# Performance work log

Hardware: AMD Instinct MI355X
Metric: run time of the kernel (lower is better)

## Reference

```python
import jax, jax.numpy as jnp
import numpy as np

KEY_DIM = 64
SCALE_PER_SEQ = 1.0 / np.sqrt(KEY_DIM).astype(np.float32)   # attn_scale_factor_per_seq default
SCALE_OVER_SEQS = 1.0 / np.sqrt(KEY_DIM).astype(np.float32) # attn_scale_factor_over_seqs default


def setup_inputs() -> dict:
    key = jax.random.key(0)
    ks = jax.random.split(key, 6)
    b, i, t, j, d = 8, 256, 64, 256, 256
    kd, vd = KEY_DIM, 64
    return {
        "input_seq": jax.random.normal(ks[0], (b, i, d), dtype=jnp.float32),
        "memory_x": jax.random.normal(ks[1], (b, t, j, d), dtype=jnp.float32),
        "memory_y": jax.random.normal(ks[2], (b, t, j, d), dtype=jnp.float32),
        "Wq": jax.random.normal(ks[3], (d, kd), dtype=jnp.float32) * (1.0 / np.sqrt(d)),
        "bq": jnp.zeros((kd,), dtype=jnp.float32),
        "Wk": jax.random.normal(ks[4], (d, kd), dtype=jnp.float32) * (1.0 / np.sqrt(d)),
        "bk": jnp.zeros((kd,), dtype=jnp.float32),
        "Wv": jax.random.normal(ks[5], (d, vd), dtype=jnp.float32) * (1.0 / np.sqrt(d)),
        "bv": jnp.zeros((vd,), dtype=jnp.float32),
    }


def reference(input_seq, memory_x, memory_y, Wq, bq, Wk, bk, Wv, bv):
    # Dense projections
    queries = input_seq @ Wq + bq            # [b, i, kd]
    keys = memory_x @ Wk + bk                # [b, t, j, kd]
    values = memory_y @ Wv + bv              # [b, t, j, vd]

    # Raw scores between every query and every token of every memory sequence
    attn_mat = jnp.einsum('bik,btjk->btij', queries, keys)  # [b, t, i, j]

    # Level 1: within-sequence attention (softmax over tokens j)
    per_seq_attn = jax.nn.softmax(SCALE_PER_SEQ * attn_mat, axis=-1)
    per_seq_retrieved = jnp.einsum('btij,btjk->btik', per_seq_attn, values)  # [b, t, i, vd]

    # Level 2: over-sequences attention (max over j, softmax over t)
    mem_seq_scores = jnp.max(attn_mat, axis=-1)                      # [b, t, i]
    mem_seq_attn = jax.nn.softmax(SCALE_OVER_SEQS * mem_seq_scores, axis=1)

    retrieved_mems = jnp.einsum('bti,btik->bik', mem_seq_attn, per_seq_retrieved)  # [b, i, vd]
    return retrieved_mems
```

## Files before the change

kernel.cpp:

```cpp
#include <hip/hip_runtime.h>
#include <hip/hip_bf16.h>

#define NB 8
#define NT 64
#define NI 256
#define NJ 256
#define ND 256
#define NKD 64
#define NVD 64
#define SCL 0.125f

typedef __attribute__((ext_vector_type(4))) float f32x4;
typedef __attribute__((ext_vector_type(8))) short bf16x8;
typedef __attribute__((ext_vector_type(4))) short bf16x4;
typedef __attribute__((ext_vector_type(4))) unsigned int uint32x4;

#define MFMA16(A, B, C) __builtin_amdgcn_mfma_f32_16x16x32_bf16((A), (B), (C), 0, 0, 0)

#define R2B 32768

__device__ __forceinline__ unsigned short f2bf(float x) {
  return __builtin_bit_cast(unsigned short, __float2bfloat16(x));
}
__device__ __forceinline__ float bf2f(unsigned short h) {
  return __builtin_bit_cast(float, (unsigned)h << 16);
}
__device__ __forceinline__ void split8(const float* __restrict__ x, bf16x8& hi, bf16x8& lo) {
  #pragma unroll
  for (int e = 0; e < 8; ++e) {
    unsigned short h = f2bf(x[e]);
    hi[e] = (short)h;
    lo[e] = (short)f2bf(x[e] - bf2f(h));
  }
}

__global__ __launch_bounds__(256) void k_prep_wt(
    const float* __restrict__ Wk, const float* __restrict__ Wv,
    unsigned short* __restrict__ Wkth,
    unsigned short* __restrict__ Wvth, unsigned short* __restrict__ Wvtl) {
  int t = blockIdx.x * 256 + threadIdx.x;
  int d = t >> 6, kd = t & 63;
  Wkth[kd * 256 + d] = f2bf(Wk[t]);
  float x = Wv[t];
  unsigned short h = f2bf(x);
  Wvth[kd * 256 + d] = h;
  Wvtl[kd * 256 + d] = f2bf(x - bf2f(h));
}

__global__ __launch_bounds__(64) void k_proj_q(
    const float* __restrict__ x, const float* __restrict__ Wq,
    const float* __restrict__ bq,
    unsigned short* __restrict__ Qh, unsigned short* __restrict__ Ql) {
  int row = blockIdx.x, lane = threadIdx.x;
  __shared__ __align__(16) float xs[ND];
  const float* xr = x + (size_t)row * ND;
  #pragma unroll
  for (int cc = 0; cc < 4; ++cc) xs[lane + 64 * cc] = xr[lane + 64 * cc];
  __syncthreads();
  float acc = bq[lane];
  #pragma unroll 4
  for (int d = 0; d < ND; ++d) acc = fmaf(xs[d], Wq[d * NKD + lane], acc);
  unsigned short h = f2bf(acc);
  Qh[(size_t)row * NKD + lane] = h;
  Ql[(size_t)row * NKD + lane] = f2bf(acc - bf2f(h));
}

__device__ __forceinline__ void stage_plane(
    char* dstb, const unsigned short* __restrict__ Wt, int tid) {
  #pragma unroll
  for (int it = 0; it < 4; ++it) {
    int qq = tid + it * 512;
    int r = qq >> 5, pb = qq & 31;
    uint4 v = *(const uint4*)((const char*)Wt + (size_t)qq * 16);
    *(uint4*)(dstb + r * 512 + ((pb ^ (r & 7)) << 4)) = v;
  }
}

__global__ __launch_bounds__(512, 4) void k_fused(
    const float* __restrict__ Xm, const float* __restrict__ Ym,
    const unsigned short* __restrict__ Wkth,
    const unsigned short* __restrict__ Wvth, const unsigned short* __restrict__ Wvtl,
    const float* __restrict__ bk, const float* __restrict__ bv,
    const unsigned short* __restrict__ Qh, const unsigned short* __restrict__ Ql,
    unsigned short* __restrict__ R,
    float* __restrict__ Sc) {
  __shared__ __align__(16) char smemb[65536];
  int tid = threadIdx.x;
  int bt = blockIdx.x, b = bt >> 6;
  int w = tid >> 6, lane = tid & 63, c = lane & 15, g = lane >> 4;

  stage_plane(smemb, Wvth, tid);
  stage_plane(smemb + R2B, Wvtl, tid);
  __syncthreads();

  f32x4 vacc[2][4];
  {
    const float* yr0 = Ym + (size_t)bt * 65536 + (size_t)(w * 32 + c) * 256 + g * 8;
    const float* yr1 = yr0 + 16 * 256;
    #pragma unroll
    for (int mf = 0; mf < 2; ++mf)
      #pragma unroll
      for (int nf = 0; nf < 4; ++nf) vacc[mf][nf] = (f32x4)0.f;
    float4 a00 = *(const float4*)(yr0),      a01 = *(const float4*)(yr0 + 4);
    float4 a10 = *(const float4*)(yr1),      a11 = *(const float4*)(yr1 + 4);
    float4 b00 = *(const float4*)(yr0 + 32), b01 = *(const float4*)(yr0 + 36);
    float4 b10 = *(const float4*)(yr1 + 32), b11 = *(const float4*)(yr1 + 36);
    #pragma unroll
    for (int ks = 0; ks < 8; ++ks) {
      float y0[8], y1[8];
      if (ks & 1) {
        *(float4*)&y0[0] = b00; *(float4*)&y0[4] = b01;
        *(float4*)&y1[0] = b10; *(float4*)&y1[4] = b11;
        if (ks < 6) {
          b00 = *(const float4*)(yr0 + (ks + 2) * 32);
          b01 = *(const float4*)(yr0 + (ks + 2) * 32 + 4);
          b10 = *(const float4*)(yr1 + (ks + 2) * 32);
          b11 = *(const float4*)(yr1 + (ks + 2) * 32 + 4);
        }
      } else {
        *(float4*)&y0[0] = a00; *(float4*)&y0[4] = a01;
        *(float4*)&y1[0] = a10; *(float4*)&y1[4] = a11;
        if (ks < 6) {
          a00 = *(const float4*)(yr0 + (ks + 2) * 32);
          a01 = *(const float4*)(yr0 + (ks + 2) * 32 + 4);
          a10 = *(const float4*)(yr1 + (ks + 2) * 32);
          a11 = *(const float4*)(yr1 + (ks + 2) * 32 + 4);
        }
      }
      bf16x8 a0h, a0l, a1h, a1l;
      split8(y0, a0h, a0l);
      split8(y1, a1h, a1l);
      #pragma unroll
      for (int nf = 0; nf < 4; ++nf) {
        int r = nf * 16 + c;
        int ba = r * 512 + (((ks * 4 + g) ^ (r & 7)) << 4);
        bf16x8 bwh = *(const bf16x8*)(smemb + ba);
        bf16x8 bwl = *(const bf16x8*)(smemb + R2B + ba);
        vacc[0][nf] = MFMA16(a0h, bwh, vacc[0][nf]);
        vacc[0][nf] = MFMA16(a0l, bwh, vacc[0][nf]);
        vacc[0][nf] = MFMA16(a0h, bwl, vacc[0][nf]);
        vacc[1][nf] = MFMA16(a1h, bwh, vacc[1][nf]);
        vacc[1][nf] = MFMA16(a1l, bwh, vacc[1][nf]);
        vacc[1][nf] = MFMA16(a1h, bwl, vacc[1][nf]);
      }
    }
  }
  __syncthreads();

  #pragma unroll
  for (int nf = 0; nf < 4; ++nf) {
    int vd = nf * 16 + c;
    float bs = bv[vd];
    #pragma unroll
    for (int mf = 0; mf < 2; ++mf) {
      bf16x4 ph;
      #pragma unroll
      for (int r = 0; r < 4; ++r) ph[r] = (short)f2bf(vacc[mf][nf][r] + bs);
      int pb = w * 4 + mf * 2 + (g >> 1);
      int ba = R2B + vd * 512 + ((pb ^ (vd & 7)) << 4) + (g & 1) * 8;
      *(bf16x4*)(smemb + ba) = ph;
    }
  }
  stage_plane(smemb, Wkth, tid);
  __syncthreads();

  f32x4 kacc[4][2];
  {
    const float* xr0 = Xm + (size_t)bt * 65536 + (size_t)(w * 32 + c) * 256 + g * 8;
    const float* xr1 = xr0 + 16 * 256;
    #pragma unroll
    for (int mf = 0; mf < 4; ++mf) { kacc[mf][0] = (f32x4)0.f; kacc[mf][1] = (f32x4)0.f; }
    float4 a00 = *(const float4*)(xr0),      a01 = *(const float4*)(xr0 + 4);
    float4 a10 = *(const float4*)(xr1),      a11 = *(const float4*)(xr1 + 4);
    float4 b00 = *(const float4*)(xr0 + 32), b01 = *(const float4*)(xr0 + 36);
    float4 b10 = *(const float4*)(xr1 + 32), b11 = *(const float4*)(xr1 + 36);
    #pragma unroll
    for (int ks = 0; ks < 8; ++ks) {
      float x0[8], x1[8];
      if (ks & 1) {
        *(float4*)&x0[0] = b00; *(float4*)&x0[4] = b01;
        *(float4*)&x1[0] = b10; *(float4*)&x1[4] = b11;
        if (ks < 6) {
          b00 = *(const float4*)(xr0 + (ks + 2) * 32);
          b01 = *(const float4*)(xr0 + (ks + 2) * 32 + 4);
          b10 = *(const float4*)(xr1 + (ks + 2) * 32);
          b11 = *(const float4*)(xr1 + (ks + 2) * 32 + 4);
        }
      } else {
        *(float4*)&x0[0] = a00; *(float4*)&x0[4] = a01;
        *(float4*)&x1[0] = a10; *(float4*)&x1[4] = a11;
        if (ks < 6) {
          a00 = *(const float4*)(xr0 + (ks + 2) * 32);
          a01 = *(const float4*)(xr0 + (ks + 2) * 32 + 4);
          a10 = *(const float4*)(xr1 + (ks + 2) * 32);
          a11 = *(const float4*)(xr1 + (ks + 2) * 32 + 4);
        }
      }
      bf16x8 b0h, b0l, b1h, b1l;
      split8(x0, b0h, b0l);
      split8(x1, b1h, b1l);
      #pragma unroll
      for (int mf = 0; mf < 4; ++mf) {
        int r = mf * 16 + c;
        int ba = r * 512 + (((ks * 4 + g) ^ (r & 7)) << 4);
        bf16x8 awh = *(const bf16x8*)(smemb + ba);
        kacc[mf][0] = MFMA16(awh, b0h, kacc[mf][0]);
        kacc[mf][0] = MFMA16(awh, b0l, kacc[mf][0]);
        kacc[mf][1] = MFMA16(awh, b1h, kacc[mf][1]);
        kacc[mf][1] = MFMA16(awh, b1l, kacc[mf][1]);
      }
    }
  }
  __syncthreads();

  #pragma unroll
  for (int nf = 0; nf < 2; ++nf) {
    int j = w * 32 + nf * 16 + c;
    #pragma unroll
    for (int mf = 0; mf < 4; ++mf) {
      bf16x4 ph;
      #pragma unroll
      for (int r = 0; r < 4; ++r)
        ph[r] = (short)f2bf(kacc[mf][nf][r] + bk[mf * 16 + g * 4 + r]);
      int pb = mf * 2 + (g >> 1);
      int ba = j * 128 + ((pb ^ (j & 7)) << 4) + (g & 1) * 8;
      *(bf16x4*)(smemb + ba) = ph;
    }
  }
  __syncthreads();

  #pragma unroll
  for (int ic = 0; ic < 2; ++ic) {
    int i = w * 32 + ic * 16 + c;
    bf16x8 qbh[2], qbl[2];
    #pragma unroll
    for (int ks = 0; ks < 2; ++ks) {
      size_t qo = ((size_t)b * NI + i) * NKD + ks * 32 + g * 8;
      qbh[ks] = *(const bf16x8*)(Qh + qo);
      qbl[ks] = *(const bf16x8*)(Ql + qo);
    }

    f32x4 sa[16];
    #pragma unroll
    for (int jf = 0; jf < 16; ++jf) sa[jf] = (f32x4)0.f;
    #pragma unroll
    for (int jf = 0; jf < 16; ++jf) {
      int j = jf * 16 + c;
      #pragma unroll
      for (int ks = 0; ks < 2; ++ks) {
        int ba = j * 128 + (((ks * 4 + g) ^ (j & 7)) << 4);
        bf16x8 kh = *(const bf16x8*)(smemb + ba);
        sa[jf] = MFMA16(kh, qbh[ks], sa[jf]);
        sa[jf] = MFMA16(kh, qbl[ks], sa[jf]);
      }
    }

    float mx = sa[0][0];
    #pragma unroll
    for (int jf = 0; jf < 16; ++jf)
      #pragma unroll
      for (int r = 0; r < 4; ++r) mx = fmaxf(mx, sa[jf][r]);
    mx = fmaxf(mx, __shfl_xor(mx, 16));
    mx = fmaxf(mx, __shfl_xor(mx, 32));
    if (g == 0) Sc[(size_t)bt * NI + i] = mx;
    float sum = 0.f;
    #pragma unroll
    for (int jf = 0; jf < 16; ++jf)
      #pragma unroll
      for (int r = 0; r < 4; ++r) {
        float p = __expf((sa[jf][r] - mx) * SCL);
        sa[jf][r] = p;
        sum += p;
      }
    sum += __shfl_xor(sum, 16);
    sum += __shfl_xor(sum, 32);
    float linv = 1.0f / sum;

    unsigned int plo[16], phi[16];
    #pragma unroll
    for (int jf = 0; jf < 16; ++jf) {
      plo[jf] = (unsigned int)f2bf(sa[jf][0]) | ((unsigned int)f2bf(sa[jf][1]) << 16);
      phi[jf] = (unsigned int)f2bf(sa[jf][2]) | ((unsigned int)f2bf(sa[jf][3]) << 16);
    }

    int srcA = c + 32 * (g & 1);
    int srcB = srcA + 16;
    bool hiH = (g >= 2);

    f32x4 racc[4];
    #pragma unroll
    for (int vf = 0; vf < 4; ++vf) racc[vf] = (f32x4)0.f;
    #pragma unroll
    for (int js = 0; js < 8; ++js) {
      int a0 = __shfl((int)plo[2 * js], srcA);
      int a1 = __shfl((int)phi[2 * js], srcA);
      int a2 = __shfl((int)plo[2 * js], srcB);
      int a3 = __shfl((int)phi[2 * js], srcB);
      int b0 = __shfl((int)plo[2 * js + 1], srcA);
      int b1 = __shfl((int)phi[2 * js + 1], srcA);
      int b2 = __shfl((int)plo[2 * js + 1], srcB);
      int b3 = __shfl((int)phi[2 * js + 1], srcB);
      uint32x4 pw;
      pw[0] = (unsigned int)(hiH ? b0 : a0);
      pw[1] = (unsigned int)(hiH ? b1 : a1);
      pw[2] = (unsigned int)(hiH ? b2 : a2);
      pw[3] = (unsigned int)(hiH ? b3 : a3);
      bf16x8 pf = __builtin_bit_cast(bf16x8, pw);
      #pragma unroll
      for (int vf = 0; vf < 4; ++vf) {
        int vd = vf * 16 + c;
        int vba = R2B + vd * 512 + (((js * 4 + g) ^ (vd & 7)) << 4);
        bf16x8 vh = *(const bf16x8*)(smemb + vba);
        racc[vf] = MFMA16(vh, pf, racc[vf]);
      }
    }

    #pragma unroll
    for (int vf = 0; vf < 4; ++vf) {
      bf16x4 rk;
      #pragma unroll
      for (int r = 0; r < 4; ++r) rk[r] = (short)f2bf(racc[vf][r] * linv);
      *(bf16x4*)(R + ((size_t)bt * NI + i) * NKD + vf * 16 + g * 4) = rk;
    }
  }
}

__global__ __launch_bounds__(64) void k_level2(
    const float* __restrict__ Sc,
    const unsigned short* __restrict__ R,
    float* __restrict__ out) {
  int bi = blockIdx.x;
  int b = bi >> 8, i = bi & 255;
  int lane = threadIdx.x;
  float sc = Sc[((size_t)b * NT + lane) * NI + i];
  float mx = sc;
  #pragma unroll
  for (int off = 32; off; off >>= 1) mx = fmaxf(mx, __shfl_xor(mx, off));
  float e = __expf((sc - mx) * SCL);
  float sum = e;
  #pragma unroll
  for (int off = 32; off; off >>= 1) sum += __shfl_xor(sum, off);
  float wn = e / sum;
  float acc = 0.f;
  for (int t = 0; t < NT; ++t) {
    float wt = __shfl(wn, t);
    acc = fmaf(wt, bf2f(R[(((size_t)b * NT + t) * NI + i) * NKD + lane]), acc);
  }
  out[((size_t)b * NI + i) * NVD + lane] = acc;
}

extern "C" void kernel_launch(void* const* d_in, const int* in_sizes, int n_in,
                              void* d_out, int out_size, void* d_ws, size_t ws_size,
                              hipStream_t stream) {
  const float* x   = (const float*)d_in[0];
  const float* mxp = (const float*)d_in[1];
  const float* myp = (const float*)d_in[2];
  const float* Wq  = (const float*)d_in[3];
  const float* bq  = (const float*)d_in[4];
  const float* Wk  = (const float*)d_in[5];
  const float* bk  = (const float*)d_in[6];
  const float* Wv  = (const float*)d_in[7];
  const float* bv  = (const float*)d_in[8];
  float* out = (float*)d_out;

  char* p = (char*)d_ws;
  auto alloc = [&](size_t bytes) { char* r = p; p += (bytes + 255) & ~(size_t)255; return r; };
  unsigned short* Qh   = (unsigned short*)alloc(2048 * 64 * 2);
  unsigned short* Ql   = (unsigned short*)alloc(2048 * 64 * 2);
  unsigned short* Rw   = (unsigned short*)alloc((size_t)131072 * 64 * 2);
  float*          Scw  = (float*)alloc((size_t)131072 * 4);
  unsigned short* Wkth = (unsigned short*)alloc(64 * 256 * 2);
  unsigned short* Wvth = (unsigned short*)alloc(64 * 256 * 2);
  unsigned short* Wvtl = (unsigned short*)alloc(64 * 256 * 2);

  hipLaunchKernelGGL(k_prep_wt, dim3(64), dim3(256), 0, stream,
                     Wk, Wv, Wkth, Wvth, Wvtl);
  hipLaunchKernelGGL(k_proj_q, dim3(NB * NI), dim3(64), 0, stream, x, Wq, bq, Qh, Ql);
  hipLaunchKernelGGL(k_fused, dim3(NB * NT), dim3(512), 0, stream,
                     mxp, myp, Wkth, Wvth, Wvtl, bk, bv, Qh, Ql, Rw, Scw);
  hipLaunchKernelGGL(k_level2, dim3(NB * NI), dim3(64), 0, stream, Scw, Rw, out);
}
```

Baseline: 98.81 us.

## Merge prep kernels, deepen global prefetch, hoist Q loads, widen level2 blocks

The weight-transpose and Q-projection kernels are merged into one launch to save a kernel launch. In the fused kernel, global loads of memory_y are issued before the weight staging barrier, memory_x loads are issued before the V write-back and K-weight staging, and the prefetch depth grows from two slices to four. Q fragments are loaded once up front instead of inside the per-row loop. The level-2 kernel now packs four rows per 256-thread block. Together these aim to hide memory latency and cut launch overhead, at the cost of more live registers at 4 blocks per CU of 512 threads, which could force spills.

```diff
diff --git a/kernel.cpp b/kernel.cpp
--- a/kernel.cpp
+++ b/kernel.cpp
@@ -34,24 +34,25 @@
   }
 }
 
-__global__ __launch_bounds__(256) void k_prep_wt(
+__global__ __launch_bounds__(64) void k_prep_projq(
+    const float* __restrict__ x, const float* __restrict__ Wq,
+    const float* __restrict__ bq,
     const float* __restrict__ Wk, const float* __restrict__ Wv,
     unsigned short* __restrict__ Wkth,
-    unsigned short* __restrict__ Wvth, unsigned short* __restrict__ Wvtl) {
-  int t = blockIdx.x * 256 + threadIdx.x;
-  int d = t >> 6, kd = t & 63;
-  Wkth[kd * 256 + d] = f2bf(Wk[t]);
-  float x = Wv[t];
-  unsigned short h = f2bf(x);
-  Wvth[kd * 256 + d] = h;
-  Wvtl[kd * 256 + d] = f2bf(x - bf2f(h));
-}
-
-__global__ __launch_bounds__(64) void k_proj_q(
-    const float* __restrict__ x, const float* __restrict__ Wq,
-    const float* __restrict__ bq,
+    unsigned short* __restrict__ Wvth, unsigned short* __restrict__ Wvtl,
     unsigned short* __restrict__ Qh, unsigned short* __restrict__ Ql) {
-  int row = blockIdx.x, lane = threadIdx.x;
+  int lane = threadIdx.x;
+  if (blockIdx.x < 256) {
+    int t = blockIdx.x * 64 + lane;
+    int d = t >> 6, kd = t & 63;
+    Wkth[kd * 256 + d] = f2bf(Wk[t]);
+    float v = Wv[t];
+    unsigned short h = f2bf(v);
+    Wvth[kd * 256 + d] = h;
+    Wvtl[kd * 256 + d] = f2bf(v - bf2f(h));
+    return;
+  }
+  int row = blockIdx.x - 256;
   __shared__ __align__(16) float xs[ND];
   const float* xr = x + (size_t)row * ND;
   #pragma unroll
@@ -89,64 +90,67 @@
   int bt = blockIdx.x, b = bt >> 6;
   int w = tid >> 6, lane = tid & 63, c = lane & 15, g = lane >> 4;
 
+  const float* yr0 = Ym + (size_t)bt * 65536 + (size_t)(w * 32 + c) * 256 + g * 8;
+  const float* yr1 = yr0 + 16 * 256;
+  const float* xr0 = Xm + (size_t)bt * 65536 + (size_t)(w * 32 + c) * 256 + g * 8;
+  const float* xr1 = xr0 + 16 * 256;
+
+  float4 pby[4][4];
+  #pragma unroll
+  for (int s = 0; s < 4; ++s) {
+    pby[s][0] = *(const float4*)(yr0 + s * 32);
+    pby[s][1] = *(const float4*)(yr0 + s * 32 + 4);
+    pby[s][2] = *(const float4*)(yr1 + s * 32);
+    pby[s][3] = *(const float4*)(yr1 + s * 32 + 4);
+  }
   stage_plane(smemb, Wvth, tid);
   stage_plane(smemb + R2B, Wvtl, tid);
   __syncthreads();
 
   f32x4 vacc[2][4];
-  {
-    const float* yr0 = Ym + (size_t)bt * 65536 + (size_t)(w * 32 + c) * 256 + g * 8;
-    const float* yr1 = yr0 + 16 * 256;
-    #pragma unroll
-    for (int mf = 0; mf < 2; ++mf)
-      #pragma unroll
-      for (int nf = 0; nf < 4; ++nf) vacc[mf][nf] = (f32x4)0.f;
-    float4 a00 = *(const float4*)(yr0),      a01 = *(const float4*)(yr0 + 4);
-    float4 a10 = *(const float4*)(yr1),      a11 = *(const float4*)(yr1 + 4);
-    float4 b00 = *(const float4*)(yr0 + 32), b01 = *(const float4*)(yr0 + 36);
-    float4 b10 = *(const float4*)(yr1 + 32), b11 = *(const float4*)(yr1 + 36);
-    #pragma unroll
-    for (int ks = 0; ks < 8; ++ks) {
-      float y0[8], y1[8];
-      if (ks & 1) {
-        *(float4*)&y0[0] = b00; *(float4*)&y0[4] = b01;
-        *(float4*)&y1[0] = b10; *(float4*)&y1[4] = b11;
-        if (ks < 6) {
-          b00 = *(const float4*)(yr0 + (ks + 2) * 32);
-          b01 = *(const float4*)(yr0 + (ks + 2) * 32 + 4);
-          b10 = *(const float4*)(yr1 + (ks + 2) * 32);
-          b11 = *(const float4*)(yr1 + (ks + 2) * 32 + 4);
-        }
-      } else {
-        *(float4*)&y0[0] = a00; *(float4*)&y0[4] = a01;
-        *(float4*)&y1[0] = a10; *(float4*)&y1[4] = a11;
-        if (ks < 6) {
-          a00 = *(const float4*)(yr0 + (ks + 2) * 32);
-          a01 = *(const float4*)(yr0 + (ks + 2) * 32 + 4);
-          a10 = *(const float4*)(yr1 + (ks + 2) * 32);
-          a11 = *(const float4*)(yr1 + (ks + 2) * 32 + 4);
-        }
-      }
-      bf16x8 a0h, a0l, a1h, a1l;
-      split8(y0, a0h, a0l);
-      split8(y1, a1h, a1l);
-      #pragma unroll
-      for (int nf = 0; nf < 4; ++nf) {
-        int r = nf * 16 + c;
-        int ba = r * 512 + (((ks * 4 + g) ^ (r & 7)) << 4);
-        bf16x8 bwh = *(const bf16x8*)(smemb + ba);
-        bf16x8 bwl = *(const bf16x8*)(smemb + R2B + ba);
-        vacc[0][nf] = MFMA16(a0h, bwh, vacc[0][nf]);
-        vacc[0][nf] = MFMA16(a0l, bwh, vacc[0][nf]);
-        vacc[0][nf] = MFMA16(a0h, bwl, vacc[0][nf]);
-        vacc[1][nf] = MFMA16(a1h, bwh, vacc[1][nf]);
-        vacc[1][nf] = MFMA16(a1l, bwh, vacc[1][nf]);
-        vacc[1][nf] = MFMA16(a1h, bwl, vacc[1][nf]);
-      }
-    }
-  }
-  __syncthreads();
-
+  #pragma unroll
+  for (int mf = 0; mf < 2; ++mf)
+    #pragma unroll
+    for (int nf = 0; nf < 4; ++nf) vacc[mf][nf] = (f32x4)0.f;
+  #pragma unroll
+  for (int ks = 0; ks < 8; ++ks) {
+    int s = ks & 3;
+    float y0[8], y1[8];
+    *(float4*)&y0[0] = pby[s][0]; *(float4*)&y0[4] = pby[s][1];
+    *(float4*)&y1[0] = pby[s][2]; *(float4*)&y1[4] = pby[s][3];
+    if (ks < 4) {
+      pby[s][0] = *(const float4*)(yr0 + (ks + 4) * 32);
+      pby[s][1] = *(const float4*)(yr0 + (ks + 4) * 32 + 4);
+      pby[s][2] = *(const float4*)(yr1 + (ks + 4) * 32);
+      pby[s][3] = *(const float4*)(yr1 + (ks + 4) * 32 + 4);
+    }
+    bf16x8 a0h, a0l, a1h, a1l;
+    split8(y0, a0h, a0l);
+    split8(y1, a1h, a1l);
+    #pragma unroll
+    for (int nf = 0; nf < 4; ++nf) {
+      int r = nf * 16 + c;
+      int ba = r * 512 + (((ks * 4 + g) ^ (r & 7)) << 4);
+      bf16x8 bwh = *(const bf16x8*)(smemb + ba);
+      bf16x8 bwl = *(const bf16x8*)(smemb + R2B + ba);
+      vacc[0][nf] = MFMA16(a0h, bwh, vacc[0][nf]);
+      vacc[0][nf] = MFMA16(a0l, bwh, vacc[0][nf]);
+      vacc[0][nf] = MFMA16(a0h, bwl, vacc[0][nf]);
+      vacc[1][nf] = MFMA16(a1h, bwh, vacc[1][nf]);
+      vacc[1][nf] = MFMA16(a1l, bwh, vacc[1][nf]);
+      vacc[1][nf] = MFMA16(a1h, bwl, vacc[1][nf]);
+    }
+  }
+  __syncthreads();
+
+  float4 pbx[4][4];
+  #pragma unroll
+  for (int s = 0; s < 4; ++s) {
+    pbx[s][0] = *(const float4*)(xr0 + s * 32);
+    pbx[s][1] = *(const float4*)(xr0 + s * 32 + 4);
+    pbx[s][2] = *(const float4*)(xr1 + s * 32);
+    pbx[s][3] = *(const float4*)(xr1 + s * 32 + 4);
+  }
   #pragma unroll
   for (int nf = 0; nf < 4; ++nf) {
     int vd = nf * 16 + c;
@@ -165,54 +169,45 @@
   __syncthreads();
 
   f32x4 kacc[4][2];
-  {
-    const float* xr0 = Xm + (size_t)bt * 65536 + (size_t)(w * 32 + c) * 256 + g * 8;
-    const float* xr1 = xr0 + 16 * 256;
-    #pragma unroll
-    for (int mf = 0; mf < 4; ++mf) { kacc[mf][0] = (f32x4)0.f; kacc[mf][1] = (f32x4)0.f; }
-    float4 a00 = *(const float4*)(xr0),      a01 = *(const float4*)(xr0 + 4);
-    float4 a10 = *(const float4*)(xr1),      a11 = *(const float4*)(xr1 + 4);
-    float4 b00 = *(const float4*)(xr0 + 32), b01 = *(const float4*)(xr0 + 36);
-    float4 b10 = *(const float4*)(xr1 + 32), b11 = *(const float4*)(xr1 + 36);
-    #pragma unroll
-    for (int ks = 0; ks < 8; ++ks) {
-      float x0[8], x1[8];
-      if (ks & 1) {
-        *(float4*)&x0[0] = b00; *(float4*)&x0[4] = b01;
-        *(float4*)&x1[0] = b10; *(float4*)&x1[4] = b11;
-        if (ks < 6) {
-          b00 = *(const float4*)(xr0 + (ks + 2) * 32);
-          b01 = *(const float4*)(xr0 + (ks + 2) * 32 + 4);
-          b10 = *(const float4*)(xr1 + (ks + 2) * 32);
-          b11 = *(const float4*)(xr1 + (ks + 2) * 32 + 4);
-        }
-      } else {
-        *(float4*)&x0[0] = a00; *(float4*)&x0[4] = a01;
-        *(float4*)&x1[0] = a10; *(float4*)&x1[4] = a11;
-        if (ks < 6) {
-          a00 = *(const float4*)(xr0 + (ks + 2) * 32);
-          a01 = *(const float4*)(xr0 + (ks + 2) * 32 + 4);
-          a10 = *(const float4*)(xr1 + (ks + 2) * 32);
-          a11 = *(const float4*)(xr1 + (ks + 2) * 32 + 4);
-        }
-      }
-      bf16x8 b0h, b0l, b1h, b1l;
-      split8(x0, b0h, b0l);
-      split8(x1, b1h, b1l);
-      #pragma unroll
-      for (int mf = 0; mf < 4; ++mf) {
-        int r = mf * 16 + c;
-        int ba = r * 512 + (((ks * 4 + g) ^ (r & 7)) << 4);
-        bf16x8 awh = *(const bf16x8*)(smemb + ba);
-        kacc[mf][0] = MFMA16(awh, b0h, kacc[mf][0]);
-        kacc[mf][0] = MFMA16(awh, b0l, kacc[mf][0]);
-        kacc[mf][1] = MFMA16(awh, b1h, kacc[mf][1]);
-        kacc[mf][1] = MFMA16(awh, b1l, kacc[mf][1]);
-      }
-    }
-  }
-  __syncthreads();
-
+  #pragma unroll
+  for (int mf = 0; mf < 4; ++mf) { kacc[mf][0] = (f32x4)0.f; kacc[mf][1] = (f32x4)0.f; }
+  #pragma unroll
+  for (int ks = 0; ks < 8; ++ks) {
+    int s = ks & 3;
+    float x0[8], x1[8];
+    *(float4*)&x0[0] = pbx[s][0]; *(float4*)&x0[4] = pbx[s][1];
+    *(float4*)&x1[0] = pbx[s][2]; *(float4*)&x1[4] = pbx[s][3];
+    if (ks < 4) {
+      pbx[s][0] = *(const float4*)(xr0 + (ks + 4) * 32);
+      pbx[s][1] = *(const float4*)(xr0 + (ks + 4) * 32 + 4);
+      pbx[s][2] = *(const float4*)(xr1 + (ks + 4) * 32);
+      pbx[s][3] = *(const float4*)(xr1 + (ks + 4) * 32 + 4);
+    }
+    bf16x8 b0h, b0l, b1h, b1l;
+    split8(x0, b0h, b0l);
+    split8(x1, b1h, b1l);
+    #pragma unroll
+    for (int mf = 0; mf < 4; ++mf) {
+      int r = mf * 16 + c;
+      int ba = r * 512 + (((ks * 4 + g) ^ (r & 7)) << 4);
+      bf16x8 awh = *(const bf16x8*)(smemb + ba);
+      kacc[mf][0] = MFMA16(awh, b0h, kacc[mf][0]);
+      kacc[mf][0] = MFMA16(awh, b0l, kacc[mf][0]);
+      kacc[mf][1] = MFMA16(awh, b1h, kacc[mf][1]);
+      kacc[mf][1] = MFMA16(awh, b1l, kacc[mf][1]);
+    }
+  }
+  __syncthreads();
+
+  bf16x8 qbh[2][2], qbl[2][2];
+  #pragma unroll
+  for (int ks = 0; ks < 2; ++ks)
+    #pragma unroll
+    for (int ic = 0; ic < 2; ++ic) {
+      size_t qo = ((size_t)b * NI + w * 32 + ic * 16 + c) * NKD + ks * 32 + g * 8;
+      qbh[ks][ic] = *(const bf16x8*)(Qh + qo);
+      qbl[ks][ic] = *(const bf16x8*)(Ql + qo);
+    }
   #pragma unroll
   for (int nf = 0; nf < 2; ++nf) {
     int j = w * 32 + nf * 16 + c;
@@ -232,13 +227,6 @@
   #pragma unroll
   for (int ic = 0; ic < 2; ++ic) {
     int i = w * 32 + ic * 16 + c;
-    bf16x8 qbh[2], qbl[2];
-    #pragma unroll
-    for (int ks = 0; ks < 2; ++ks) {
-      size_t qo = ((size_t)b * NI + i) * NKD + ks * 32 + g * 8;
-      qbh[ks] = *(const bf16x8*)(Qh + qo);
-      qbl[ks] = *(const bf16x8*)(Ql + qo);
-    }
 
     f32x4 sa[16];
     #pragma unroll
@@ -250,8 +238,8 @@
       for (int ks = 0; ks < 2; ++ks) {
         int ba = j * 128 + (((ks * 4 + g) ^ (j & 7)) << 4);
         bf16x8 kh = *(const bf16x8*)(smemb + ba);
-        sa[jf] = MFMA16(kh, qbh[ks], sa[jf]);
-        sa[jf] = MFMA16(kh, qbl[ks], sa[jf]);
+        sa[jf] = MFMA16(kh, qbh[ks][ic], sa[jf]);
+        sa[jf] = MFMA16(kh, qbl[ks][ic], sa[jf]);
       }
     }
 
@@ -325,13 +313,13 @@
   }
 }
 
-__global__ __launch_bounds__(64) void k_level2(
+__global__ __launch_bounds__(256) void k_level2(
     const float* __restrict__ Sc,
     const unsigned short* __restrict__ R,
     float* __restrict__ out) {
-  int bi = blockIdx.x;
+  int w = threadIdx.x >> 6, lane = threadIdx.x & 63;
+  int bi = blockIdx.x * 4 + w;
   int b = bi >> 8, i = bi & 255;
-  int lane = threadIdx.x;
   float sc = Sc[((size_t)b * NT + lane) * NI + i];
   float mx = sc;
   #pragma unroll
@@ -373,10 +361,9 @@
   unsigned short* Wvth = (unsigned short*)alloc(64 * 256 * 2);
   unsigned short* Wvtl = (unsigned short*)alloc(64 * 256 * 2);
 
-  hipLaunchKernelGGL(k_prep_wt, dim3(64), dim3(256), 0, stream,
-                     Wk, Wv, Wkth, Wvth, Wvtl);
-  hipLaunchKernelGGL(k_proj_q, dim3(NB * NI), dim3(64), 0, stream, x, Wq, bq, Qh, Ql);
+  hipLaunchKernelGGL(k_prep_projq, dim3(256 + NB * NI), dim3(64), 0, stream,
+                     x, Wq, bq, Wk, Wv, Wkth, Wvth, Wvtl, Qh, Ql);
   hipLaunchKernelGGL(k_fused, dim3(NB * NT), dim3(512), 0, stream,
                      mxp, myp, Wkth, Wvth, Wvtl, bk, bv, Qh, Ql, Rw, Scw);
-  hipLaunchKernelGGL(k_level2, dim3(NB * NI), dim3(64), 0, stream, Scw, Rw, out);
-}
+  hipLaunchKernelGGL(k_level2, dim3(512), dim3(256), 0, stream, Scw, Rw, out);
+}
```

New measurement: 96.59 us. -2.2%, faster.
